# Kernel tuning notes

Measured on AMD Instinct MI355X. Metric: run time of the kernel, lower is better.

Reference implementation:

```python
import jax, jax.numpy as jnp
import numpy as np

N_NODES = 50000
N_EDGES = 800000
IN_FEATS = 32
OUT_FEATS = 32
NUM_HEADS = 4


def setup_inputs() -> dict:
    key = jax.random.key(0)
    ks = jax.random.split(key, 12)
    H, F, IN = NUM_HEADS, OUT_FEATS, IN_FEATS
    h = jax.random.normal(ks[0], (N_NODES, IN), dtype=jnp.float32)
    src = jax.random.randint(ks[1], (N_EDGES,), 0, N_NODES, dtype=jnp.int64)
    dst = jax.random.randint(ks[2], (N_EDGES,), 0, N_NODES, dtype=jnp.int64)
    s = 0.1
    W_gat = jax.random.normal(ks[3], (IN, H * F), dtype=jnp.float32) * s
    attn_l = jax.random.normal(ks[4], (H, F), dtype=jnp.float32) * s
    attn_r = jax.random.normal(ks[5], (H, F), dtype=jnp.float32) * s
    W_ih = jax.random.normal(ks[6], (3 * F, H * F), dtype=jnp.float32) * s
    W_hh = jax.random.normal(ks[7], (3 * F, F), dtype=jnp.float32) * s
    b_ih = jax.random.normal(ks[8], (3 * F,), dtype=jnp.float32) * s
    b_hh = jax.random.normal(ks[9], (3 * F,), dtype=jnp.float32) * s
    return {"h": h, "W_gat": W_gat, "attn_l": attn_l, "attn_r": attn_r,
            "W_ih": W_ih, "W_hh": W_hh, "b_ih": b_ih, "b_hh": b_hh,
            "src": src, "dst": dst}


def reference(h, W_gat, attn_l, attn_r, W_ih, W_hh, b_ih, b_hh, src, dst):
    N = h.shape[0]
    H, F = attn_l.shape
    # --- GATConv ---
    feat = (h @ W_gat).reshape(N, H, F)                      # (N,H,F)
    el = jnp.einsum('nhf,hf->nh', feat, attn_l)              # (N,H)
    er = jnp.einsum('nhf,hf->nh', feat, attn_r)              # (N,H)
    e = jax.nn.leaky_relu(el[src] + er[dst], 0.2)            # (E,H) edge logits
    emax = jax.ops.segment_max(e, dst, num_segments=N)       # per-dst max (stable)
    ee = jnp.exp(e - emax[dst])
    denom = jax.ops.segment_sum(ee, dst, num_segments=N)
    alpha = ee / denom[dst]                                  # segment softmax (E,H)
    msg = feat[src] * alpha[:, :, None]                      # (E,H,F)
    agg = jax.ops.segment_sum(msg, dst, num_segments=N)      # (N,H,F)
    x = agg.reshape(N, H * F)
    # --- GRUCell (torch semantics, gate order r,z,n) ---
    gi = x @ W_ih.T + b_ih                                   # (N,3F)
    gh = h @ W_hh.T + b_hh                                   # (N,3F)
    i_r, i_z, i_n = jnp.split(gi, 3, axis=1)
    h_r, h_z, h_n = jnp.split(gh, 3, axis=1)
    r = jax.nn.sigmoid(i_r + h_r)
    z = jax.nn.sigmoid(i_z + h_z)
    n = jnp.tanh(i_n + r * h_n)
    h_new = (1.0 - z) * n + z * h
    return jax.nn.elu(h_new)
```

## Files before the change

### kernel.cpp

```cpp
#include <hip/hip_runtime.h>
#include <hip/hip_bf16.h>
#include <cmath>

#define N_NODES 50000
#define N_EDGES 800000
#define CAP 64

#define NBINS 196
#define BIN_CAP 8192
#define CUR_PAD 32

#define P1_EPT 16
#define P1_EPB (1024 * P1_EPT)
#define P1_BLOCKS ((N_EDGES + P1_EPB - 1) / P1_EPB)

#define HB_BLOCKS 98
#define ELR_BLOCKS 196
#define WC_BLOCKS 30
#define NB_HB  (P1_BLOCKS)
#define NB_ELR (NB_HB + HB_BLOCKS)
#define NB_WC  (NB_ELR + ELR_BLOCKS)
#define NB_WGB (NB_WC + WC_BLOCKS)
#define PREP_TOTAL (NB_WGB + 1)

#define AGGR_BLOCKS (N_NODES / 16)

typedef __attribute__((ext_vector_type(8))) short bf16x8;
typedef __attribute__((ext_vector_type(4))) float f32x4;

__device__ inline short bfbits(float x) {
    __hip_bfloat16 t = __float2bfloat16(x);
    return *reinterpret_cast<short*>(&t);
}
__device__ inline unsigned short bfu16(float x) {
    __hip_bfloat16 t = __float2bfloat16(x);
    return *reinterpret_cast<unsigned short*>(&t);
}

__global__ __launch_bounds__(1024) void k_part_prep(
        const int* __restrict__ src, const int* __restrict__ dst,
        int* __restrict__ bin_cursor, unsigned* __restrict__ bin_buf,
        const float* __restrict__ h, const float* __restrict__ Wg,
        const float* __restrict__ al, const float* __restrict__ ar,
        const float* __restrict__ Wih, const float* __restrict__ Whh,
        unsigned short* __restrict__ hb, float* __restrict__ el,
        float* __restrict__ er, __hip_bfloat16* __restrict__ Wc,
        __hip_bfloat16* __restrict__ Wgb) {
    const int t = threadIdx.x;
    __shared__ union {
        struct {
            int bcnt[256], bofs[256], cur[256], gbase[256];
            int wt4[4];
            unsigned stage[P1_EPB];
        } part;
        __hip_bfloat16 vlr[16][32];
    } sm;

    if (blockIdx.x < P1_BLOCKS) {
        int* bcnt = sm.part.bcnt; int* bofs = sm.part.bofs;
        int* cur = sm.part.cur;   int* gbase = sm.part.gbase;
        int* wt4 = sm.part.wt4;   unsigned* stage = sm.part.stage;
        if (t < 256) bcnt[t] = 0;
        __syncthreads();
        int bn[P1_EPT];
        unsigned pk[P1_EPT];
        const int ebase = blockIdx.x * P1_EPB + t * P1_EPT;
        if (ebase < N_EDGES) {
            int dd[P1_EPT], ss[P1_EPT];
#pragma unroll
            for (int q = 0; q < P1_EPT / 4; ++q) {
                *(int4*)(dd + q * 4) = *(const int4*)(dst + ebase + q * 4);
                *(int4*)(ss + q * 4) = *(const int4*)(src + ebase + q * 4);
            }
#pragma unroll
            for (int q = 0; q < P1_EPT; ++q) {
                bn[q] = dd[q] >> 8;
                pk[q] = (unsigned)ss[q] | ((unsigned)dd[q] << 16);
                atomicAdd(&bcnt[bn[q]], 1);
            }
        } else {
#pragma unroll
            for (int q = 0; q < P1_EPT; ++q) bn[q] = -1;
        }
        __syncthreads();
        int x = 0, vv = 0;
        if (t < 256) {
            vv = bcnt[t];
            x = vv;
            const int lane = t & 63;
#pragma unroll
            for (int m = 1; m < 64; m <<= 1) {
                const int y = __shfl_up(x, m, 64);
                if (lane >= m) x += y;
            }
            if (lane == 63) wt4[t >> 6] = x;
        }
        __syncthreads();
        if (t < 256) {
            const int wave4 = t >> 6;
            int wb = 0;
#pragma unroll
            for (int i = 0; i < 4; ++i) if (i < wave4) wb += wt4[i];
            const int off = wb + x - vv;
            bofs[t] = off;
            cur[t] = off;
            gbase[t] = (vv > 0) ? atomicAdd(&bin_cursor[t * CUR_PAD], vv) : 0;
        }
        __syncthreads();
        if (bn[0] >= 0) {
#pragma unroll
            for (int q = 0; q < P1_EPT; ++q)
                stage[atomicAdd(&cur[bn[q]], 1)] = pk[q];
        }
        __syncthreads();
        const int tot = wt4[0] + wt4[1] + wt4[2] + wt4[3];
        for (int i = t; i < tot; i += 1024) {
            const unsigned e = stage[i];
            const int b = e >> 24;
            const int gi = gbase[b] + (i - bofs[b]);
            if (gi < BIN_CAP) bin_buf[(size_t)b * BIN_CAP + gi] = e;
        }
        return;
    }
    if (blockIdx.x < NB_ELR) {
        const int idx = (blockIdx.x - NB_HB) * 1024 + t;
        const int base = idx * 16;
        if (base < N_NODES * 32) {
            const float4* hp = (const float4*)(h + base);
            const float4 v0 = hp[0], v1 = hp[1], v2 = hp[2], v3 = hp[3];
            unsigned o[8];
            o[0] = (unsigned)bfu16(v0.x) | ((unsigned)bfu16(v0.y) << 16);
            o[1] = (unsigned)bfu16(v0.z) | ((unsigned)bfu16(v0.w) << 16);
            o[2] = (unsigned)bfu16(v1.x) | ((unsigned)bfu16(v1.y) << 16);
            o[3] = (unsigned)bfu16(v1.z) | ((unsigned)bfu16(v1.w) << 16);
            o[4] = (unsigned)bfu16(v2.x) | ((unsigned)bfu16(v2.y) << 16);
            o[5] = (unsigned)bfu16(v2.z) | ((unsigned)bfu16(v2.w) << 16);
            o[6] = (unsigned)bfu16(v3.x) | ((unsigned)bfu16(v3.y) << 16);
            o[7] = (unsigned)bfu16(v3.z) | ((unsigned)bfu16(v3.w) << 16);
            uint4* op = (uint4*)(hb + base);
            op[0] = (uint4){o[0], o[1], o[2], o[3]};
            op[1] = (uint4){o[4], o[5], o[6], o[7]};
        }
        return;
    }
    if (blockIdx.x < NB_WC) {
        if (t < 512) {
            const int col = t >> 5, k = t & 31;
            float v = 0.f;
            if (col < 8) {
                const int hd = col & 3;
                const float* a = (col < 4) ? (al + hd * 32) : (ar + hd * 32);
                const float* w = Wg + k * 128 + hd * 32;
#pragma unroll
                for (int f = 0; f < 32; ++f) v = fmaf(w[f], a[f], v);
            }
            sm.vlr[col][k] = __float2bfloat16(v);
        }
        __syncthreads();
        const int wave = t >> 6, lane = t & 63;
        const int li = lane & 15, quad = lane >> 4;
        const int mt = (blockIdx.x - NB_ELR) * 16 + wave;
        if (mt >= AGGR_BLOCKS) return;
        const int m_base = mt * 16;
        bf16x8 a;
        {
            const float4* hp = (const float4*)(h + (size_t)(m_base + li) * 32 + quad * 8);
            const float4 f0 = hp[0], f1 = hp[1];
            a[0] = bfbits(f0.x); a[1] = bfbits(f0.y); a[2] = bfbits(f0.z); a[3] = bfbits(f0.w);
            a[4] = bfbits(f1.x); a[5] = bfbits(f1.y); a[6] = bfbits(f1.z); a[7] = bfbits(f1.w);
        }
        const bf16x8 b = *(const bf16x8*)(&sm.vlr[li][0] + quad * 8);
        f32x4 acc = (f32x4){0.f, 0.f, 0.f, 0.f};
        acc = __builtin_amdgcn_mfma_f32_16x16x32_bf16(a, b, acc, 0, 0, 0);
        if (li < 8) {
#pragma unroll
            for (int i = 0; i < 4; ++i) {
                const int m = m_base + quad * 4 + i;
                if (li < 4) el[m * 4 + li] = acc[i];
                else        er[m * 4 + (li - 4)] = acc[i];
            }
        }
        return;
    }
    if (blockIdx.x < NB_WGB) {
        const int idx = (blockIdx.x - NB_WC) * 1024 + t;
        const int r = idx / 160, k = idx - r * 160;
        float v = 0.f;
        if (r < 96) { if (k < 128) v = Wih[r * 128 + k]; }
        else        { if (k >= 128) v = Whh[(r - 96) * 32 + (k - 128)]; }
        Wc[idx] = __float2bfloat16(v);
        return;
    }
#pragma unroll
    for (int jj = 0; jj < 4; ++jj) {
        const int id = t * 4 + jj;
        const int k = id & 31, f = (id >> 5) & 31, hd = id >> 10;
        Wgb[id] = __float2bfloat16(Wg[k * 128 + hd * 32 + f]);
    }
}

__global__ __launch_bounds__(256) void k_aggr_gru(
        const int* __restrict__ bin_cursor, const unsigned* __restrict__ bin_buf,
        const unsigned char* __restrict__ hb,
        const float* __restrict__ el, const float* __restrict__ er,
        const float* __restrict__ h, const __hip_bfloat16* __restrict__ Wc,
        const __hip_bfloat16* __restrict__ Wgb,
        const float* __restrict__ bih, const float* __restrict__ bhh,
        float* __restrict__ out) {
    __shared__ unsigned short list[16][CAP];
    __shared__ int lcnt[16];
    __shared__ __hip_bfloat16 xh_tile[16][160];
    __shared__ float eel_s[4][256];
    __shared__ unsigned Sn[16][64];
    __shared__ float ex[2][3][16][16];
    const int t = threadIdx.x;
    const int wave = t >> 6;
    const int lane = t & 63;
    const int pb = blockIdx.x >> 4, six = blockIdx.x & 15;
    const int mbase = blockIdx.x * 16;

    if (t < 16) lcnt[t] = 0;
    __syncthreads();

    const int cbn = min(bin_cursor[pb * CUR_PAD], BIN_CAP);
    const uint4* bb4 = (const uint4*)(bin_buf + (size_t)pb * BIN_CAP);
    for (int i = t * 4; i < cbn; i += 1024) {
        const uint4 p4 = bb4[i >> 2];
#pragma unroll
        for (int k = 0; k < 4; ++k) {
            if (i + k < cbn) {
                const unsigned p = (&p4.x)[k];
                const int local = (p >> 16) & 255;
                if ((local >> 4) == six) {
                    const int dl = local & 15;
                    const int pos = atomicAdd(&lcnt[dl], 1);
                    if (pos < CAP) list[dl][pos] = (unsigned short)(p & 0xffff);
                }
            }
        }
    }
    __syncthreads();

    float* eel = eel_s[wave];
    const int hs = lane & 3;
    const int eq = lane >> 4;
    const int dw = lane & 15;
    for (int u = 0; u < 4; ++u) {
        const int row = wave * 4 + u;
        const int n = mbase + row;
        const float ern = er[n * 4 + hs];
        const int cnt = min(lcnt[row], CAP);
        const unsigned short* sl = list[row];
        eel[lane] = 0.f; eel[64 + lane] = 0.f;
        eel[128 + lane] = 0.f; eel[192 + lane] = 0.f;
        __builtin_amdgcn_wave_barrier();
        float psum = 0.f;
#pragma unroll
        for (int p = 0; p < 4; ++p) {
            const int j = p * 64 + lane;
            if (j < cnt * 4) {
                const int s = sl[j >> 2];
                float v = el[s * 4 + hs] + ern;
                v = v > 0.f ? v : 0.2f * v;
                const float e = __expf(v);
                eel[j] = e;
                psum += e;
            }
        }
        __builtin_amdgcn_wave_barrier();
        float a00 = 0.f, a01 = 0.f, a10 = 0.f, a11 = 0.f;
        float a20 = 0.f, a21 = 0.f, a30 = 0.f, a31 = 0.f;
        for (int i = 0; i < cnt; i += 16) {
            int e[4];
#pragma unroll
            for (int j = 0; j < 4; ++j) {
                const int ee = i + j * 4 + eq;
                e[j] = (ee < cnt) ? sl[ee] : 0;
            }
            unsigned q[4];
#pragma unroll
            for (int j = 0; j < 4; ++j)
                q[j] = *(const unsigned*)(hb + (size_t)e[j] * 64 + dw * 4);
#pragma unroll
            for (int j = 0; j < 4; ++j) {
                const int ee = i + j * 4 + eq;
                const float lo = __uint_as_float(q[j] << 16);
                const float hi = __uint_as_float(q[j] & 0xffff0000u);
                const float w0 = eel[ee * 4 + 0];
                const float w1 = eel[ee * 4 + 1];
                const float w2 = eel[ee * 4 + 2];
                const float w3 = eel[ee * 4 + 3];
                a00 = fmaf(w0, lo, a00); a01 = fmaf(w0, hi, a01);
                a10 = fmaf(w1, lo, a10); a11 = fmaf(w1, hi, a11);
                a20 = fmaf(w2, lo, a20); a21 = fmaf(w2, hi, a21);
                a30 = fmaf(w3, lo, a30); a31 = fmaf(w3, hi, a31);
            }
        }
        __builtin_amdgcn_wave_barrier();
#pragma unroll
        for (int m = 16; m < 64; m <<= 1) {
            a00 += __shfl_xor(a00, m, 64); a01 += __shfl_xor(a01, m, 64);
            a10 += __shfl_xor(a10, m, 64); a11 += __shfl_xor(a11, m, 64);
            a20 += __shfl_xor(a20, m, 64); a21 += __shfl_xor(a21, m, 64);
            a30 += __shfl_xor(a30, m, 64); a31 += __shfl_xor(a31, m, 64);
        }
#pragma unroll
        for (int m = 4; m < 64; m <<= 1) psum += __shfl_xor(psum, m, 64);
        const float inv0 = (cnt > 0) ? 1.f / __shfl(psum, 0, 64) : 0.f;
        const float inv1 = (cnt > 0) ? 1.f / __shfl(psum, 1, 64) : 0.f;
        const float inv2 = (cnt > 0) ? 1.f / __shfl(psum, 2, 64) : 0.f;
        const float inv3 = (cnt > 0) ? 1.f / __shfl(psum, 3, 64) : 0.f;
        if (lane < 16) {
            Sn[row][0 * 16 + lane] = (unsigned)bfu16(a00 * inv0) | ((unsigned)bfu16(a01 * inv0) << 16);
            Sn[row][1 * 16 + lane] = (unsigned)bfu16(a10 * inv1) | ((unsigned)bfu16(a11 * inv1) << 16);
            Sn[row][2 * 16 + lane] = (unsigned)bfu16(a20 * inv2) | ((unsigned)bfu16(a21 * inv2) << 16);
            Sn[row][3 * 16 + lane] = (unsigned)bfu16(a30 * inv3) | ((unsigned)bfu16(a31 * inv3) << 16);
        }
        if (lane < 32)
            xh_tile[row][128 + lane] = __float2bfloat16(h[(size_t)n * 32 + lane]);
    }
    __syncthreads();

    {
        const int li = lane & 15, quad = lane >> 4;
        const int head = wave;
        const __hip_bfloat16* snb = (const __hip_bfloat16*)&Sn[0][0];
        const bf16x8 aS = *(const bf16x8*)(snb + li * 128 + head * 32 + quad * 8);
        const bf16x8 b0 = *(const bf16x8*)(Wgb + (size_t)(head * 32 + li) * 32 + quad * 8);
        const bf16x8 b1 = *(const bf16x8*)(Wgb + (size_t)(head * 32 + 16 + li) * 32 + quad * 8);
        f32x4 c0 = (f32x4){0.f, 0.f, 0.f, 0.f};
        f32x4 c1 = (f32x4){0.f, 0.f, 0.f, 0.f};
        c0 = __builtin_amdgcn_mfma_f32_16x16x32_bf16(aS, b0, c0, 0, 0, 0);
        c1 = __builtin_amdgcn_mfma_f32_16x16x32_bf16(aS, b1, c1, 0, 0, 0);
#pragma unroll
        for (int i = 0; i < 4; ++i) {
            const int row = quad * 4 + i;
            xh_tile[row][head * 32 + li]      = __float2bfloat16(c0[i]);
            xh_tile[row][head * 32 + 16 + li] = __float2bfloat16(c1[i]);
        }
    }
    __syncthreads();

    const int li = lane & 15, quad = lane >> 4;
    const int cb = wave >> 1;
    const int ghrole = wave & 1;
    bf16x8 a[5];
#pragma unroll
    for (int s = 0; s < 5; ++s)
        a[s] = *(const bf16x8*)((const char*)&xh_tile[0][0] + li * 320 + s * 64 + quad * 16);
    f32x4 acc[3];
#pragma unroll
    for (int g = 0; g < 3; ++g) {
        acc[g] = (f32x4){0.f, 0.f, 0.f, 0.f};
        const int j = g * 2 + cb + ghrole * 6;
        const bf16x8* bp = (const bf16x8*)(Wc + (size_t)(j * 16 + li) * 160 + quad * 8);
        acc[g] = __builtin_amdgcn_mfma_f32_16x16x32_bf16(a[0], bp[0],  acc[g], 0, 0, 0);
        acc[g] = __builtin_amdgcn_mfma_f32_16x16x32_bf16(a[1], bp[4],  acc[g], 0, 0, 0);
        acc[g] = __builtin_amdgcn_mfma_f32_16x16x32_bf16(a[2], bp[8],  acc[g], 0, 0, 0);
        acc[g] = __builtin_amdgcn_mfma_f32_16x16x32_bf16(a[3], bp[12], acc[g], 0, 0, 0);
        acc[g] = __builtin_amdgcn_mfma_f32_16x16x32_bf16(a[4], bp[16], acc[g], 0, 0, 0);
    }
    if (ghrole) {
#pragma unroll
        for (int g = 0; g < 3; ++g)
#pragma unroll
            for (int i = 0; i < 4; ++i)
                ex[cb][g][quad * 4 + i][li] = acc[g][i];
    }
    __syncthreads();
    if (!ghrole) {
        const int c = cb * 16 + li;
        const float bir = bih[c],      bhr = bhh[c];
        const float biz = bih[32 + c], bhz = bhh[32 + c];
        const float bin = bih[64 + c], bhn = bhh[64 + c];
#pragma unroll
        for (int i = 0; i < 4; ++i) {
            const int row = quad * 4 + i;
            const int m = mbase + row;
            const float gr = acc[0][i] + bir + ex[cb][0][row][li] + bhr;
            const float gz = acc[1][i] + biz + ex[cb][1][row][li] + bhz;
            const float r = 1.f / (1.f + __expf(-gr));
            const float z = 1.f / (1.f + __expf(-gz));
            const float tv = acc[2][i] + bin + r * (ex[cb][2][row][li] + bhn);
            const float em = __expf(-2.f * fabsf(tv));
            const float nn = copysignf((1.f - em) / (1.f + em), tv);
            const float hv = h[(size_t)m * 32 + c];
            const float hn = (1.f - z) * nn + z * hv;
            out[(size_t)m * 32 + c] = hn > 0.f ? hn : (__expf(hn) - 1.f);
        }
    }
}

extern "C" void kernel_launch(void* const* d_in, const int* in_sizes, int n_in,
                              void* d_out, int out_size, void* d_ws, size_t ws_size,
                              hipStream_t stream) {
    const float* h   = (const float*)d_in[0];
    const float* Wg  = (const float*)d_in[1];
    const float* al  = (const float*)d_in[2];
    const float* ar  = (const float*)d_in[3];
    const float* Wih = (const float*)d_in[4];
    const float* Whh = (const float*)d_in[5];
    const float* bih = (const float*)d_in[6];
    const float* bhh = (const float*)d_in[7];
    const int* src   = (const int*)d_in[8];
    const int* dst   = (const int*)d_in[9];
    float* out = (float*)d_out;

    unsigned short* hb = (unsigned short*)d_ws;
    unsigned* bin_buf = (unsigned*)(hb + (size_t)N_NODES * 32);
    float* el = (float*)(bin_buf + (size_t)NBINS * BIN_CAP);
    float* er = el + (size_t)N_NODES * 4;
    __hip_bfloat16* Wc  = (__hip_bfloat16*)(er + (size_t)N_NODES * 4);
    __hip_bfloat16* Wgb = Wc + 30720;
    int* bin_cursor = (int*)(Wgb + 4096);

    hipMemsetAsync(bin_cursor, 0, NBINS * CUR_PAD * sizeof(int), stream);
    k_part_prep<<<PREP_TOTAL, 1024, 0, stream>>>(
        src, dst, bin_cursor, bin_buf, h, Wg, al, ar, Wih, Whh,
        hb, el, er, Wc, Wgb);
    k_aggr_gru<<<AGGR_BLOCKS, 256, 0, stream>>>(
        bin_cursor, bin_buf, (const unsigned char*)hb, el, er, h, Wc, Wgb,
        bih, bhh, out);
}
```

Before: 142.1 us.

## Add per-bin scatter kernel building CSR lists; pack el into padded bf16 feature rows

Adds a new kernel that scatters each bin's packed edges once into per-node fixed-capacity source lists with counts. The aggregation kernel then loads its 16 rows directly instead of having 16 blocks each rescan the whole bin. The el logits are stored as bf16 next to each node's bf16 features in a padded 40-element row, so one gather fetches both. This costs an extra launch plus a global write and read of the lists, and lowers el to bf16 precision.

```diff
diff --git a/kernel.cpp b/kernel.cpp
--- a/kernel.cpp
+++ b/kernel.cpp
@@ -13,6 +13,8 @@
 #define P1_EPT 16
 #define P1_EPB (1024 * P1_EPT)
 #define P1_BLOCKS ((N_EDGES + P1_EPB - 1) / P1_EPB)
+
+#define HROW 40
 
 #define HB_BLOCKS 98
 #define ELR_BLOCKS 196
@@ -43,9 +45,8 @@
         const float* __restrict__ h, const float* __restrict__ Wg,
         const float* __restrict__ al, const float* __restrict__ ar,
         const float* __restrict__ Wih, const float* __restrict__ Whh,
-        unsigned short* __restrict__ hb, float* __restrict__ el,
-        float* __restrict__ er, __hip_bfloat16* __restrict__ Wc,
-        __hip_bfloat16* __restrict__ Wgb) {
+        unsigned short* __restrict__ hb, float* __restrict__ er,
+        __hip_bfloat16* __restrict__ Wc, __hip_bfloat16* __restrict__ Wgb) {
     const int t = threadIdx.x;
     __shared__ union {
         struct {
@@ -124,9 +125,9 @@
     }
     if (blockIdx.x < NB_ELR) {
         const int idx = (blockIdx.x - NB_HB) * 1024 + t;
-        const int base = idx * 16;
-        if (base < N_NODES * 32) {
-            const float4* hp = (const float4*)(h + base);
+        const int n = idx >> 1, half = idx & 1;
+        if (n < N_NODES) {
+            const float4* hp = (const float4*)(h + (size_t)n * 32 + half * 16);
             const float4 v0 = hp[0], v1 = hp[1], v2 = hp[2], v3 = hp[3];
             unsigned o[8];
             o[0] = (unsigned)bfu16(v0.x) | ((unsigned)bfu16(v0.y) << 16);
@@ -137,7 +138,7 @@
             o[5] = (unsigned)bfu16(v2.z) | ((unsigned)bfu16(v2.w) << 16);
             o[6] = (unsigned)bfu16(v3.x) | ((unsigned)bfu16(v3.y) << 16);
             o[7] = (unsigned)bfu16(v3.z) | ((unsigned)bfu16(v3.w) << 16);
-            uint4* op = (uint4*)(hb + base);
+            uint4* op = (uint4*)(hb + (size_t)n * HROW + half * 16);
             op[0] = (uint4){o[0], o[1], o[2], o[3]};
             op[1] = (uint4){o[4], o[5], o[6], o[7]};
         }
@@ -176,8 +177,10 @@
 #pragma unroll
             for (int i = 0; i < 4; ++i) {
                 const int m = m_base + quad * 4 + i;
-                if (li < 4) el[m * 4 + li] = acc[i];
-                else        er[m * 4 + (li - 4)] = acc[i];
+                if (li < 4)
+                    ((__hip_bfloat16*)hb)[(size_t)m * HROW + 32 + li] = __float2bfloat16(acc[i]);
+                else
+                    er[m * 4 + (li - 4)] = acc[i];
             }
         }
         return;
@@ -199,10 +202,38 @@
     }
 }
 
+__global__ __launch_bounds__(256) void k_scat2(
+        const int* __restrict__ bin_cursor, const unsigned* __restrict__ bin_buf,
+        unsigned short* __restrict__ srcs_p, int* __restrict__ counts) {
+    __shared__ int lcnt[256];
+    const int t = threadIdx.x;
+    const int b = blockIdx.x;
+    lcnt[t] = 0;
+    __syncthreads();
+    const int cb = min(bin_cursor[b * CUR_PAD], BIN_CAP);
+    const uint4* bb4 = (const uint4*)(bin_buf + (size_t)b * BIN_CAP);
+    for (int i = t * 4; i < cb; i += 1024) {
+        const uint4 p4 = bb4[i >> 2];
+#pragma unroll
+        for (int k = 0; k < 4; ++k) {
+            if (i + k < cb) {
+                const unsigned p = (&p4.x)[k];
+                const int dl = (p >> 16) & 255;
+                const int pos = atomicAdd(&lcnt[dl], 1);
+                if (pos < CAP)
+                    srcs_p[(size_t)(b * 256 + dl) * CAP + pos] = (unsigned short)(p & 0xffff);
+            }
+        }
+    }
+    __syncthreads();
+    const int node = b * 256 + t;
+    if (node < N_NODES) counts[node] = lcnt[t];
+}
+
 __global__ __launch_bounds__(256) void k_aggr_gru(
-        const int* __restrict__ bin_cursor, const unsigned* __restrict__ bin_buf,
-        const unsigned char* __restrict__ hb,
-        const float* __restrict__ el, const float* __restrict__ er,
+        const int* __restrict__ counts, const unsigned short* __restrict__ srcs_p,
+        const unsigned short* __restrict__ hb,
+        const float* __restrict__ er,
         const float* __restrict__ h, const __hip_bfloat16* __restrict__ Wc,
         const __hip_bfloat16* __restrict__ Wgb,
         const float* __restrict__ bih, const float* __restrict__ bhh,
@@ -216,28 +247,12 @@
     const int t = threadIdx.x;
     const int wave = t >> 6;
     const int lane = t & 63;
-    const int pb = blockIdx.x >> 4, six = blockIdx.x & 15;
     const int mbase = blockIdx.x * 16;
 
-    if (t < 16) lcnt[t] = 0;
-    __syncthreads();
-
-    const int cbn = min(bin_cursor[pb * CUR_PAD], BIN_CAP);
-    const uint4* bb4 = (const uint4*)(bin_buf + (size_t)pb * BIN_CAP);
-    for (int i = t * 4; i < cbn; i += 1024) {
-        const uint4 p4 = bb4[i >> 2];
-#pragma unroll
-        for (int k = 0; k < 4; ++k) {
-            if (i + k < cbn) {
-                const unsigned p = (&p4.x)[k];
-                const int local = (p >> 16) & 255;
-                if ((local >> 4) == six) {
-                    const int dl = local & 15;
-                    const int pos = atomicAdd(&lcnt[dl], 1);
-                    if (pos < CAP) list[dl][pos] = (unsigned short)(p & 0xffff);
-                }
-            }
-        }
+    if (t < 16) lcnt[t] = min(counts[mbase + t], CAP);
+    {
+        const ushort4* sp = (const ushort4*)(srcs_p + (size_t)mbase * CAP);
+        ((ushort4*)&list[0][0])[t] = sp[t];
     }
     __syncthreads();
 
@@ -249,7 +264,7 @@
         const int row = wave * 4 + u;
         const int n = mbase + row;
         const float ern = er[n * 4 + hs];
-        const int cnt = min(lcnt[row], CAP);
+        const int cnt = lcnt[row];
         const unsigned short* sl = list[row];
         eel[lane] = 0.f; eel[64 + lane] = 0.f;
         eel[128 + lane] = 0.f; eel[192 + lane] = 0.f;
@@ -260,7 +275,9 @@
             const int j = p * 64 + lane;
             if (j < cnt * 4) {
                 const int s = sl[j >> 2];
-                float v = el[s * 4 + hs] + ern;
+                const float elv = __bfloat162float(
+                    *(const __hip_bfloat16*)(hb + (size_t)s * HROW + 32 + hs));
+                float v = elv + ern;
                 v = v > 0.f ? v : 0.2f * v;
                 const float e = __expf(v);
                 eel[j] = e;
@@ -275,12 +292,12 @@
 #pragma unroll
             for (int j = 0; j < 4; ++j) {
                 const int ee = i + j * 4 + eq;
-                e[j] = (ee < cnt) ? sl[ee] : 0;
+                e[j] = (ee < cnt) ? sl[ee] : sl[0];
             }
             unsigned q[4];
 #pragma unroll
             for (int j = 0; j < 4; ++j)
-                q[j] = *(const unsigned*)(hb + (size_t)e[j] * 64 + dw * 4);
+                q[j] = *(const unsigned*)(hb + (size_t)e[j] * HROW + dw * 2);
 #pragma unroll
             for (int j = 0; j < 4; ++j) {
                 const int ee = i + j * 4 + eq;
@@ -407,9 +424,10 @@
     float* out = (float*)d_out;
 
     unsigned short* hb = (unsigned short*)d_ws;
-    unsigned* bin_buf = (unsigned*)(hb + (size_t)N_NODES * 32);
-    float* el = (float*)(bin_buf + (size_t)NBINS * BIN_CAP);
-    float* er = el + (size_t)N_NODES * 4;
+    unsigned* bin_buf = (unsigned*)(hb + (size_t)N_NODES * HROW);
+    unsigned short* srcs_p = (unsigned short*)(bin_buf + (size_t)NBINS * BIN_CAP);
+    int* counts = (int*)(srcs_p + (size_t)N_NODES * CAP);
+    float* er = (float*)(counts + N_NODES);
     __hip_bfloat16* Wc  = (__hip_bfloat16*)(er + (size_t)N_NODES * 4);
     __hip_bfloat16* Wgb = Wc + 30720;
     int* bin_cursor = (int*)(Wgb + 4096);
@@ -417,8 +435,8 @@
     hipMemsetAsync(bin_cursor, 0, NBINS * CUR_PAD * sizeof(int), stream);
     k_part_prep<<<PREP_TOTAL, 1024, 0, stream>>>(
         src, dst, bin_cursor, bin_buf, h, Wg, al, ar, Wih, Whh,
-        hb, el, er, Wc, Wgb);
+        hb, er, Wc, Wgb);
+    k_scat2<<<NBINS, 256, 0, stream>>>(bin_cursor, bin_buf, srcs_p, counts);
     k_aggr_gru<<<AGGR_BLOCKS, 256, 0, stream>>>(
-        bin_cursor, bin_buf, (const unsigned char*)hb, el, er, h, Wc, Wgb,
-        bih, bhh, out);
-}
+        counts, srcs_p, hb, er, h, Wc, Wgb, bih, bhh, out);
+}
```

After: 140.2 us. No clear change (-1.4%).
